# Performance work log

Hardware: AMD Instinct MI355X
Metric: run time of the kernel (lower is better)

Reference implementation:

```python
import jax, jax.numpy as jnp
import numpy as np

EPS_DIST = 1e-10
BN_EPS = 1e-5
K = 3


def setup_inputs() -> dict:
    key = jax.random.key(0)
    ks = jax.random.split(key, 8)
    B, N1, N2, C1, C2 = 16, 4096, 1024, 128, 256
    inp = {
        "xyz1": jax.random.normal(ks[0], (B, N1, 3), jnp.float32),
        "xyz2": jax.random.normal(ks[1], (B, N2, 3), jnp.float32),
        "points1": jax.random.normal(ks[2], (B, C1, N1), jnp.float32),
        "points2": jax.random.normal(ks[3], (B, C2, N2), jnp.float32),
        "W0": jax.random.normal(ks[4], (256, C1 + C2), jnp.float32) * 0.05,
        "b0": jax.random.normal(ks[5], (256,), jnp.float32) * 0.05,
        "g0": jnp.ones((256,), jnp.float32),
        "be0": jnp.zeros((256,), jnp.float32),
        "W1": jax.random.normal(ks[6], (128, 256), jnp.float32) * 0.05,
        "b1": jax.random.normal(ks[7], (128,), jnp.float32) * 0.05,
        "g1": jnp.ones((128,), jnp.float32),
        "be1": jnp.zeros((128,), jnp.float32),
    }
    return inp


def _conv_bn_relu(x, W, b, g, beta):
    # 1x1 Conv1d == channel matmul; BN in training mode (biased batch stats over B,N)
    x = jnp.einsum("oc,bcn->bon", W, x) + b[None, :, None]
    m = jnp.mean(x, axis=(0, 2), keepdims=True)
    v = jnp.var(x, axis=(0, 2), keepdims=True)
    x = g[None, :, None] * (x - m) * jax.lax.rsqrt(v + BN_EPS) + beta[None, :, None]
    return jax.nn.relu(x)


def reference(xyz1, xyz2, points1, points2, W0, b0, g0, be0, W1, b1, g1, be1):
    B, N1, _ = xyz1.shape
    # squared pairwise distances [B, N1, N2]
    d = (
        jnp.sum(xyz1 ** 2, -1)[:, :, None]
        + jnp.sum(xyz2 ** 2, -1)[:, None, :]
        - 2.0 * jnp.einsum("bnd,bmd->bnm", xyz1, xyz2)
    )
    d = jnp.maximum(d, EPS_DIST)
    neg, idx = jax.lax.top_k(-d, K)  # smallest K
    dist = -neg  # [B, N1, K]
    w = 1.0 / dist
    w = w / jnp.sum(w, axis=-1, keepdims=True)
    # gather neighbor features: [B, N1, K, C2]
    gathered = points2[jnp.arange(B)[:, None, None], :, idx]
    interp = jnp.einsum("bnkc,bnk->bcn", gathered, w)  # [B, C2, N1]
    x = jnp.concatenate([points1, interp], axis=1)  # [B, C1+C2, N1]
    x = _conv_bn_relu(x, W0, b0, g0, be0)
    x = _conv_bn_relu(x, W1, b1, g1, be1)
    return x
```

## Files before the change

kernel.cpp:

```cpp
#include <hip/hip_runtime.h>

#define EPS_DIST 1e-10f
#define BN_EPS 1e-5f

typedef short short8 __attribute__((ext_vector_type(8)));
typedef float floatx4 __attribute__((ext_vector_type(4)));

__device__ __forceinline__ unsigned short f2bf(float f) {
  unsigned u = __float_as_uint(f);
  unsigned r = (u + 0x7FFFu + ((u >> 16) & 1u)) >> 16;
  return (unsigned short)r;
}
__device__ __forceinline__ float bf2f(unsigned short h) {
  return __uint_as_float(((unsigned)h) << 16);
}

__device__ __forceinline__ void gload16(const void* g, void* l) {
  __builtin_amdgcn_global_load_lds(
      (const __attribute__((address_space(1))) unsigned int*)g,
      (__attribute__((address_space(3))) unsigned int*)l, 16, 0, 0);
}

__global__ __launch_bounds__(256) void tcvt_all_kernel(
    const float* __restrict__ p2, unsigned short* __restrict__ Xt2,
    const float* __restrict__ p1, unsigned short* __restrict__ Xt1,
    const float* __restrict__ W0, const float* __restrict__ W1,
    unsigned short* __restrict__ Wb) {
  const int tid = threadIdx.x;
  const int id = blockIdx.x;
  if (id >= 3072) {
    int base = (id - 3072) * 2048 + tid;
#pragma unroll
    for (int p = 0; p < 8; ++p) {
      int i = base + p * 256;
      float v = (i < 98304) ? W0[i] : W1[i - 98304];
      Wb[i] = f2bf(v);
    }
    return;
  }
  __shared__ float sm[64][65];
  const float* src; unsigned short* dst; int K, N, n0, k0, b;
  if (id < 1024) {
    src = p2; dst = Xt2; K = 256; N = 1024;
    n0 = (id & 15) * 64; k0 = ((id >> 4) & 3) * 64; b = id >> 6;
  } else {
    int q = id - 1024;
    src = p1; dst = Xt1; K = 128; N = 4096;
    n0 = (q & 63) * 64; k0 = ((q >> 6) & 1) * 64; b = q >> 7;
  }
  const int nl = tid & 63, kq = tid >> 6;
  const float* s = src + ((size_t)b * K + k0) * N + n0;
#pragma unroll
  for (int p = 0; p < 16; ++p) {
    int kl = p * 4 + kq;
    sm[kl][nl] = s[(size_t)kl * N + nl];
  }
  __syncthreads();
#pragma unroll
  for (int p = 0; p < 2; ++p) {
    int c = p * 256 + tid;
    int rn = c >> 3, jj = c & 7;
    short8 v;
#pragma unroll
    for (int u = 0; u < 8; ++u) v[u] = (short)f2bf(sm[jj * 8 + u][rn]);
    *(short8*)(dst + (size_t)(b * N + n0 + rn) * K + k0 + jj * 8) = v;
  }
}

__global__ __launch_bounds__(256) void knni_kernel(
    const float* __restrict__ xyz1, const float* __restrict__ xyz2,
    const unsigned short* __restrict__ Xt2, unsigned short* __restrict__ Xi) {
  __shared__ float4 s2[1024];
  __shared__ int sidx[96];
  __shared__ float swgt[96];
  const int lin = blockIdx.x;
  const int xcd = lin & 7;
  const int slot = lin >> 3;
  const int b = xcd * 2 + (slot >> 7);
  const int qtile = slot & 127;
  const int tid = threadIdx.x;
  const float* x2 = xyz2 + b * 3072;
  for (int j = tid; j < 1024; j += 256) {
    float x = x2[j * 3 + 0], y = x2[j * 3 + 1], z = x2[j * 3 + 2];
    s2[j] = make_float4(x, y, z, (x * x + y * y) + z * z);
  }
  __syncthreads();
  const int q = tid >> 3, sub = tid & 7;
  const int n = qtile * 32 + q;
  const float* p1 = xyz1 + (b * 4096 + n) * 3;
  const float ax = p1[0], ay = p1[1], az = p1[2];
  const float s1 = (ax * ax + ay * ay) + az * az;
  float d0 = 3.4e38f, d1 = 3.4e38f, d2 = 3.4e38f;
  int i0 = 0x7fffffff, i1 = 0x7fffffff, i2 = 0x7fffffff;
#pragma unroll 8
  for (int jj = 0; jj < 128; ++jj) {
    int j = jj * 8 + sub;
    float4 c = s2[j];
    float dot = (ax * c.x + ay * c.y) + az * c.z;
    float d = fmaxf((s1 + c.w) - 2.0f * dot, EPS_DIST);
    bool c0 = d < d0, c1 = d < d1, c2 = d < d2;
    int ni0 = c0 ? j : i0;
    int ni1 = c0 ? i0 : (c1 ? j : i1);
    int ni2 = c1 ? i1 : (c2 ? j : i2);
    float nd0 = fminf(d0, d);
    float nd1 = __builtin_amdgcn_fmed3f(d0, d, d1);
    float nd2 = __builtin_amdgcn_fmed3f(d1, d, d2);
    d0 = nd0; d1 = nd1; d2 = nd2;
    i0 = ni0; i1 = ni1; i2 = ni2;
  }
#pragma unroll
  for (int m = 1; m <= 4; m <<= 1) {
    float e0 = __shfl_xor(d0, m), e1 = __shfl_xor(d1, m), e2 = __shfl_xor(d2, m);
    int   f0 = __shfl_xor(i0, m), f1 = __shfl_xor(i1, m), f2 = __shfl_xor(i2, m);
    float A[3] = {d0, d1, d2}, Bv[3] = {e0, e1, e2};
    int   I[3] = {i0, i1, i2}, J[3] = {f0, f1, f2};
    float md[3]; int mi[3];
    int pa = 0, pb = 0;
#pragma unroll
    for (int k = 0; k < 3; ++k) {
      float da = A[pa], db = Bv[pb];
      int ia = I[pa], ib = J[pb];
      bool ta = (da < db) || (da == db && ia < ib);
      md[k] = ta ? da : db; mi[k] = ta ? ia : ib;
      pa += ta ? 1 : 0; pb += ta ? 0 : 1;
    }
    d0 = md[0]; d1 = md[1]; d2 = md[2];
    i0 = mi[0]; i1 = mi[1]; i2 = mi[2];
  }
  if (sub == 0) {
    float w0 = 1.0f / d0, w1 = 1.0f / d1, w2 = 1.0f / d2;
    float s = (w0 + w1) + w2;
    sidx[q * 3 + 0] = i0; sidx[q * 3 + 1] = i1; sidx[q * 3 + 2] = i2;
    swgt[q * 3 + 0] = w0 / s; swgt[q * 3 + 1] = w1 / s; swgt[q * 3 + 2] = w2 / s;
  }
  __syncthreads();
  const int w = tid >> 6, lane = tid & 63;
  const unsigned short* zb = Xt2 + (size_t)b * 1024 * 256;
#pragma unroll
  for (int t = 0; t < 8; ++t) {
    int nl = w * 8 + t;
    int nn = qtile * 32 + nl;
    int g0 = sidx[nl * 3 + 0], g1 = sidx[nl * 3 + 1], g2 = sidx[nl * 3 + 2];
    float w0 = swgt[nl * 3 + 0], w1 = swgt[nl * 3 + 1], w2 = swgt[nl * 3 + 2];
    ushort4 r0 = *(const ushort4*)(zb + (size_t)g0 * 256 + lane * 4);
    ushort4 r1 = *(const ushort4*)(zb + (size_t)g1 * 256 + lane * 4);
    ushort4 r2 = *(const ushort4*)(zb + (size_t)g2 * 256 + lane * 4);
    ushort4 o;
    o.x = f2bf(w0 * bf2f(r0.x) + w1 * bf2f(r1.x) + w2 * bf2f(r2.x));
    o.y = f2bf(w0 * bf2f(r0.y) + w1 * bf2f(r1.y) + w2 * bf2f(r2.y));
    o.z = f2bf(w0 * bf2f(r0.z) + w1 * bf2f(r1.z) + w2 * bf2f(r2.z));
    o.w = f2bf(w0 * bf2f(r0.w) + w1 * bf2f(r1.w) + w2 * bf2f(r2.w));
    *(ushort4*)(Xi + ((size_t)b * 4096 + nn) * 256 + lane * 4) = o;
  }
}

__global__ __launch_bounds__(256) void gemm0_kernel(
    const unsigned short* __restrict__ Wb, const unsigned short* __restrict__ Xt1,
    const unsigned short* __restrict__ Xi, const float* __restrict__ b0,
    unsigned short* __restrict__ y0t, float* __restrict__ acc0x) {
  __shared__ short sA[2][128 * 32];
  __shared__ short sB[2][128 * 32];
  __shared__ float ls[256];
  const int lin = blockIdx.x;
  const int xcd = lin & 7;
  const int slot = lin >> 3;
  const int b = xcd * 2 + (slot >> 6);
  const int inner = slot & 63;
  const int o0 = (inner & 1) * 128;
  const int n0 = (inner >> 1) * 128;
  const int tid = threadIdx.x, lane = tid & 63, w = tid >> 6;
  const int wo = w >> 1, wn = w & 1, quad = lane >> 4, l15 = lane & 15;
  const int c0 = tid, c1 = 256 + tid;
  const int r0 = c0 >> 2, j0 = c0 & 3, r1 = c1 >> 2, j1 = c1 & 3;
  const unsigned short* xb = Xt1 + (size_t)(b * 4096 + n0) * 128;
  const unsigned short* xi = Xi + (size_t)(b * 4096 + n0) * 256;
  ls[tid] = 0.f;
  auto STAGE = [&](int h, int kb) {
    gload16(Wb + (size_t)(o0 + r0) * 384 + kb + j0 * 8, &sA[h][c0 * 8]);
    gload16(Wb + (size_t)(o0 + r1) * 384 + kb + j1 * 8, &sA[h][c1 * 8]);
    if (kb < 128) {
      gload16(xb + (size_t)r0 * 128 + kb + j0 * 8, &sB[h][c0 * 8]);
      gload16(xb + (size_t)r1 * 128 + kb + j1 * 8, &sB[h][c1 * 8]);
    } else {
      gload16(xi + (size_t)r0 * 256 + (kb - 128) + j0 * 8, &sB[h][c0 * 8]);
      gload16(xi + (size_t)r1 * 256 + (kb - 128) + j1 * 8, &sB[h][c1 * 8]);
    }
  };
  floatx4 acc[4][4] = {};
  STAGE(0, 0);
  asm volatile("s_waitcnt vmcnt(0)" ::: "memory");
  __syncthreads();
  int cur = 0;
  for (int t = 0; t < 12; ++t) {
    if (t < 11) STAGE(cur ^ 1, (t + 1) * 32);
    short8 av[4], bv[4];
#pragma unroll
    for (int i = 0; i < 4; ++i)
      av[i] = *(const short8*)(&sA[cur][(wo * 64 + i * 16 + l15) * 32 + quad * 8]);
#pragma unroll
    for (int j = 0; j < 4; ++j)
      bv[j] = *(const short8*)(&sB[cur][(wn * 64 + j * 16 + l15) * 32 + quad * 8]);
#pragma unroll
    for (int i = 0; i < 4; ++i)
#pragma unroll
      for (int j = 0; j < 4; ++j)
        acc[i][j] = __builtin_amdgcn_mfma_f32_16x16x32_bf16(av[i], bv[j], acc[i][j], 0, 0, 0);
    if (t < 11) {
      asm volatile("s_waitcnt vmcnt(0)" ::: "memory");
      __syncthreads();
      cur ^= 1;
    }
  }
#pragma unroll
  for (int i = 0; i < 4; ++i) {
    int obg = o0 + wo * 64 + i * 16 + quad * 4;
    floatx4 bias = *(const floatx4*)(b0 + obg);
    float ps[4] = {0.f, 0.f, 0.f, 0.f}, pq[4] = {0.f, 0.f, 0.f, 0.f};
#pragma unroll
    for (int j = 0; j < 4; ++j) {
      int n = n0 + wn * 64 + j * 16 + l15;
      ushort4 out;
      out.x = f2bf(acc[i][j][0] + bias[0]);
      out.y = f2bf(acc[i][j][1] + bias[1]);
      out.z = f2bf(acc[i][j][2] + bias[2]);
      out.w = f2bf(acc[i][j][3] + bias[3]);
      *(ushort4*)(y0t + (size_t)(b * 4096 + n) * 256 + obg) = out;
      float q0 = bf2f(out.x), q1 = bf2f(out.y), q2 = bf2f(out.z), q3 = bf2f(out.w);
      ps[0] += q0; ps[1] += q1; ps[2] += q2; ps[3] += q3;
      pq[0] += q0 * q0; pq[1] += q1 * q1; pq[2] += q2 * q2; pq[3] += q3 * q3;
    }
#pragma unroll
    for (int m = 1; m <= 8; m <<= 1) {
#pragma unroll
      for (int u = 0; u < 4; ++u) {
        ps[u] += __shfl_xor(ps[u], m);
        pq[u] += __shfl_xor(pq[u], m);
      }
    }
    if (l15 == 0) {
      int lo = obg - o0;
#pragma unroll
      for (int u = 0; u < 4; ++u) {
        atomicAdd(&ls[lo + u], ps[u]);
        atomicAdd(&ls[128 + lo + u], pq[u]);
      }
    }
  }
  __syncthreads();
  if (tid < 128) {
    atomicAdd(&acc0x[xcd * 512 + o0 + tid], ls[tid]);
    atomicAdd(&acc0x[xcd * 512 + 256 + o0 + tid], ls[128 + tid]);
  }
}

__global__ __launch_bounds__(256) void gemm1_kernel(
    const unsigned short* __restrict__ Wb, const unsigned short* __restrict__ y0t,
    const float* __restrict__ acc0x, const float* __restrict__ g0,
    const float* __restrict__ be0, const float* __restrict__ b1,
    float* __restrict__ y1, float* __restrict__ acc1x) {
  __shared__ short sA[2][128 * 32];
  __shared__ short sB[2][128 * 32];
  __shared__ float sst[512];
  __shared__ float ls[256];
  const int lin = blockIdx.x;
  const int xcd = lin & 7;
  const int slot = lin >> 3;
  const int b = xcd * 2 + (slot >> 5);
  const int n0 = (slot & 31) * 128;
  const int tid = threadIdx.x, lane = tid & 63, w = tid >> 6;
  const int wm = w & 1, wo2 = w >> 1, quad = lane >> 4, l15 = lane & 15;
  const unsigned short* W1b = Wb + 98304;
  const int c0 = tid, c1 = 256 + tid;
  const int r0 = c0 >> 2, j0 = c0 & 3, r1 = c1 >> 2, j1 = c1 & 3;
  const unsigned short* yb = y0t + (size_t)(b * 4096 + n0) * 256;
  short8 ra0, ra1;
  auto LOADRAW = [&](int kb) {
    ra0 = *(const short8*)(yb + (size_t)r0 * 256 + kb + j0 * 8);
    ra1 = *(const short8*)(yb + (size_t)r1 * 256 + kb + j1 * 8);
  };
  auto XFORM = [&](int h, int kb) {
    int k0b = kb + j0 * 8, k1b = kb + j1 * 8;
    short8 v0, v1;
#pragma unroll
    for (int u = 0; u < 8; ++u) {
      float t0 = fmaxf(bf2f((unsigned short)ra0[u]) * sst[k0b + u] + sst[256 + k0b + u], 0.f);
      float t1 = fmaxf(bf2f((unsigned short)ra1[u]) * sst[k1b + u] + sst[256 + k1b + u], 0.f);
      v0[u] = (short)f2bf(t0);
      v1[u] = (short)f2bf(t1);
    }
    *(short8*)(&sA[h][c0 * 8]) = v0;
    *(short8*)(&sA[h][c1 * 8]) = v1;
  };
  auto STAGEB = [&](int h, int kb) {
    gload16(W1b + (size_t)r0 * 256 + kb + j0 * 8, &sB[h][c0 * 8]);
    gload16(W1b + (size_t)r1 * 256 + kb + j1 * 8, &sB[h][c1 * 8]);
  };
  LOADRAW(0);
  {
    const float inv = 1.0f / 65536.0f;
    float s0 = 0.f, s1 = 0.f;
#pragma unroll
    for (int x = 0; x < 8; ++x) {
      s0 += acc0x[x * 512 + tid];
      s1 += acc0x[x * 512 + 256 + tid];
    }
    float mean = s0 * inv;
    float var = s1 * inv - mean * mean;
    float sc = g0[tid] / sqrtf(var + BN_EPS);
    sst[tid] = sc;
    sst[256 + tid] = be0[tid] - mean * sc;
  }
  ls[tid] = 0.f;
  __syncthreads();
  XFORM(0, 0);
  STAGEB(0, 0);
  asm volatile("s_waitcnt vmcnt(0)" ::: "memory");
  __syncthreads();
  floatx4 acc[4][4] = {};
  int cur = 0;
  for (int t = 0; t < 8; ++t) {
    if (t < 7) {
      LOADRAW((t + 1) * 32);
      STAGEB(cur ^ 1, (t + 1) * 32);
    }
    short8 av[4], bv[4];
#pragma unroll
    for (int i = 0; i < 4; ++i)
      av[i] = *(const short8*)(&sA[cur][(wm * 64 + i * 16 + l15) * 32 + quad * 8]);
#pragma unroll
    for (int j = 0; j < 4; ++j)
      bv[j] = *(const short8*)(&sB[cur][(wo2 * 64 + j * 16 + l15) * 32 + quad * 8]);
#pragma unroll
    for (int i = 0; i < 4; ++i)
#pragma unroll
      for (int j = 0; j < 4; ++j)
        acc[i][j] = __builtin_amdgcn_mfma_f32_16x16x32_bf16(av[i], bv[j], acc[i][j], 0, 0, 0);
    if (t < 7) {
      XFORM(cur ^ 1, (t + 1) * 32);
      asm volatile("s_waitcnt vmcnt(0)" ::: "memory");
      __syncthreads();
      cur ^= 1;
    }
  }
#pragma unroll
  for (int j = 0; j < 4; ++j) {
    int o = wo2 * 64 + j * 16 + l15;
    float bias = b1[o];
    float s = 0.f, q = 0.f;
#pragma unroll
    for (int i = 0; i < 4; ++i) {
      int n = n0 + wm * 64 + i * 16 + quad * 4;
      floatx4 v = acc[i][j] + bias;
      *(floatx4*)(y1 + (size_t)(b * 128 + o) * 4096 + n) = v;
      s += (v[0] + v[1]) + (v[2] + v[3]);
      q += (v[0] * v[0] + v[1] * v[1]) + (v[2] * v[2] + v[3] * v[3]);
    }
    s += __shfl_xor(s, 16); s += __shfl_xor(s, 32);
    q += __shfl_xor(q, 16); q += __shfl_xor(q, 32);
    if (quad == 0) {
      atomicAdd(&ls[o], s);
      atomicAdd(&ls[128 + o], q);
    }
  }
  __syncthreads();
  if (tid < 128) {
    atomicAdd(&acc1x[xcd * 256 + tid], ls[tid]);
    atomicAdd(&acc1x[xcd * 256 + 128 + tid], ls[128 + tid]);
  }
}

__global__ __launch_bounds__(256) void bnrelu_f_kernel(
    float* __restrict__ y, const float* __restrict__ acc1x,
    const float* __restrict__ g1, const float* __restrict__ be1) {
  size_t i4 = (size_t)blockIdx.x * 256 + threadIdx.x;
  int o = (int)(blockIdx.x >> 2) & 127;
  const float inv = 1.0f / 65536.0f;
  float s0 = 0.f, s1 = 0.f;
#pragma unroll
  for (int x = 0; x < 8; ++x) {
    s0 += acc1x[x * 256 + o];
    s1 += acc1x[x * 256 + 128 + o];
  }
  float m = s0 * inv;
  float var = s1 * inv - m * m;
  float sc = g1[o] / sqrtf(var + BN_EPS);
  float bb = be1[o];
  floatx4 v = ((floatx4*)y)[i4];
  floatx4 r;
  r[0] = fmaxf((v[0] - m) * sc + bb, 0.f);
  r[1] = fmaxf((v[1] - m) * sc + bb, 0.f);
  r[2] = fmaxf((v[2] - m) * sc + bb, 0.f);
  r[3] = fmaxf((v[3] - m) * sc + bb, 0.f);
  ((floatx4*)y)[i4] = r;
}

extern "C" void kernel_launch(void* const* d_in, const int* in_sizes, int n_in,
                              void* d_out, int out_size, void* d_ws, size_t ws_size,
                              hipStream_t stream) {
  (void)in_sizes; (void)n_in; (void)out_size; (void)ws_size;
  const float* xyz1    = (const float*)d_in[0];
  const float* xyz2    = (const float*)d_in[1];
  const float* points1 = (const float*)d_in[2];
  const float* points2 = (const float*)d_in[3];
  const float* W0  = (const float*)d_in[4];
  const float* b0  = (const float*)d_in[5];
  const float* g0  = (const float*)d_in[6];
  const float* be0 = (const float*)d_in[7];
  const float* W1  = (const float*)d_in[8];
  const float* b1  = (const float*)d_in[9];
  const float* g1  = (const float*)d_in[10];
  const float* be1 = (const float*)d_in[11];

  char* ws = (char*)d_ws;
  float* acc0x = (float*)(ws + 0);
  float* acc1x = (float*)(ws + 16384);
  unsigned short* Wb  = (unsigned short*)(ws + 1581056);
  unsigned short* Xt2 = (unsigned short*)(ws + 2097152);
  unsigned short* Xt1 = (unsigned short*)(ws + 10485760);
  unsigned short* y0t = (unsigned short*)(ws + 27262976);
  unsigned short* Xi = (unsigned short*)d_out;
  float* y1 = (float*)d_out;

  hipMemsetAsync(acc0x, 0, 24576, stream);
  tcvt_all_kernel<<<3136, 256, 0, stream>>>(points2, Xt2, points1, Xt1, W0, W1, Wb);
  knni_kernel<<<2048, 256, 0, stream>>>(xyz1, xyz2, Xt2, Xi);
  gemm0_kernel<<<1024, 256, 0, stream>>>(Wb, Xt1, Xi, b0, y0t, acc0x);
  gemm1_kernel<<<512, 256, 0, stream>>>(Wb, y0t, acc0x, g0, be0, b1, y1, acc1x);
  bnrelu_f_kernel<<<8192, 256, 0, stream>>>(y1, acc1x, g1, be1);
}
```

Baseline: 222.1 us.

## Triple-buffer LDS staging in both GEMM kernels with one barrier per step

After: 217.0 us. 2.3% less time.

```diff
diff --git a/kernel.cpp b/kernel.cpp
--- a/kernel.cpp
+++ b/kernel.cpp
@@ -158,8 +158,8 @@
     const unsigned short* __restrict__ Wb, const unsigned short* __restrict__ Xt1,
     const unsigned short* __restrict__ Xi, const float* __restrict__ b0,
     unsigned short* __restrict__ y0t, float* __restrict__ acc0x) {
-  __shared__ short sA[2][128 * 32];
-  __shared__ short sB[2][128 * 32];
+  __shared__ short sA[3][128 * 32];
+  __shared__ short sB[3][128 * 32];
   __shared__ float ls[256];
   const int lin = blockIdx.x;
   const int xcd = lin & 7;
@@ -188,11 +188,14 @@
   };
   floatx4 acc[4][4] = {};
   STAGE(0, 0);
-  asm volatile("s_waitcnt vmcnt(0)" ::: "memory");
-  __syncthreads();
-  int cur = 0;
+  STAGE(1, 32);
+  asm volatile("s_waitcnt lgkmcnt(0)" ::: "memory");
+  int cur = 0, nx = 2;
   for (int t = 0; t < 12; ++t) {
-    if (t < 11) STAGE(cur ^ 1, (t + 1) * 32);
+    if (t < 11) asm volatile("s_waitcnt vmcnt(4)" ::: "memory");
+    else        asm volatile("s_waitcnt vmcnt(0)" ::: "memory");
+    __builtin_amdgcn_s_barrier();
+    __builtin_amdgcn_sched_barrier(0);
     short8 av[4], bv[4];
 #pragma unroll
     for (int i = 0; i < 4; ++i)
@@ -205,11 +208,9 @@
 #pragma unroll
       for (int j = 0; j < 4; ++j)
         acc[i][j] = __builtin_amdgcn_mfma_f32_16x16x32_bf16(av[i], bv[j], acc[i][j], 0, 0, 0);
-    if (t < 11) {
-      asm volatile("s_waitcnt vmcnt(0)" ::: "memory");
-      __syncthreads();
-      cur ^= 1;
-    }
+    if (t < 10) STAGE(nx, (t + 2) * 32);
+    cur = (cur == 2) ? 0 : cur + 1;
+    nx = (nx == 2) ? 0 : nx + 1;
   }
 #pragma unroll
   for (int i = 0; i < 4; ++i) {
@@ -258,8 +259,8 @@
     const float* __restrict__ acc0x, const float* __restrict__ g0,
     const float* __restrict__ be0, const float* __restrict__ b1,
     float* __restrict__ y1, float* __restrict__ acc1x) {
-  __shared__ short sA[2][128 * 32];
-  __shared__ short sB[2][128 * 32];
+  __shared__ short sA[3][128 * 32];
+  __shared__ short sB[3][128 * 32];
   __shared__ float sst[512];
   __shared__ float ls[256];
   const int lin = blockIdx.x;
@@ -312,17 +313,18 @@
   }
   ls[tid] = 0.f;
   __syncthreads();
+  STAGEB(0, 0);
+  STAGEB(1, 32);
   XFORM(0, 0);
-  STAGEB(0, 0);
-  asm volatile("s_waitcnt vmcnt(0)" ::: "memory");
-  __syncthreads();
+  LOADRAW(32);
+  asm volatile("s_waitcnt lgkmcnt(0)" ::: "memory");
   floatx4 acc[4][4] = {};
-  int cur = 0;
+  int cur = 0, nx = 2;
   for (int t = 0; t < 8; ++t) {
-    if (t < 7) {
-      LOADRAW((t + 1) * 32);
-      STAGEB(cur ^ 1, (t + 1) * 32);
-    }
+    if (t < 7) asm volatile("s_waitcnt vmcnt(4)" ::: "memory");
+    else       asm volatile("s_waitcnt vmcnt(0)" ::: "memory");
+    __builtin_amdgcn_s_barrier();
+    __builtin_amdgcn_sched_barrier(0);
     short8 av[4], bv[4];
 #pragma unroll
     for (int i = 0; i < 4; ++i)
@@ -335,12 +337,15 @@
 #pragma unroll
       for (int j = 0; j < 4; ++j)
         acc[i][j] = __builtin_amdgcn_mfma_f32_16x16x32_bf16(av[i], bv[j], acc[i][j], 0, 0, 0);
+    if (t < 6) STAGEB(nx, (t + 2) * 32);
     if (t < 7) {
-      XFORM(cur ^ 1, (t + 1) * 32);
-      asm volatile("s_waitcnt vmcnt(0)" ::: "memory");
-      __syncthreads();
-      cur ^= 1;
-    }
+      int nxt1 = (cur == 2) ? 0 : cur + 1;
+      XFORM(nxt1, (t + 1) * 32);
+      if (t < 6) LOADRAW((t + 2) * 32);
+      asm volatile("s_waitcnt lgkmcnt(0)" ::: "memory");
+    }
+    cur = (cur == 2) ? 0 : cur + 1;
+    nx = (nx == 2) ? 0 : nx + 1;
   }
 #pragma unroll
   for (int j = 0; j < 4; ++j) {
```
